# Kernel tuning notes

Hardware: AMD Instinct MI355X
Metric: run time of the kernel (lower is better)

## Reference

```python
import jax, jax.numpy as jnp
import numpy as np

B = 16384          # batch size
NNZ_PER = 32       # active features per position (pieces)
NNZ = B * NNZ_PER
FT_OUT = 512
F_BIG = 49152
F_SMALL = 768
MOD = 640


def setup_inputs() -> dict:
    key = jax.random.key(0)
    ks = jax.random.split(key, 8)
    rows = jnp.repeat(jnp.arange(NNZ // NNZ_PER, dtype=jnp.int64), NNZ_PER)
    stm_cols = jax.random.randint(ks[0], (NNZ,), 0, F_BIG, dtype=jnp.int64)
    nstm_cols = jax.random.randint(ks[1], (NNZ,), 0, F_BIG, dtype=jnp.int64)
    stm_indices = jnp.stack([rows, stm_cols])   # [2, nnz] COO (row, col)
    nstm_indices = jnp.stack([rows, nstm_cols])
    values = jnp.ones((NNZ,), dtype=jnp.float32)
    s = 0.01
    W_ft = jax.random.normal(ks[2], (FT_OUT, F_BIG), dtype=jnp.float32) * s
    b_ft = jax.random.normal(ks[3], (FT_OUT,), dtype=jnp.float32) * s
    W_fft = jax.random.normal(ks[4], (FT_OUT, F_SMALL), dtype=jnp.float32) * s
    b_fft = jax.random.normal(ks[5], (FT_OUT,), dtype=jnp.float32) * s
    W_out = jax.random.normal(ks[6], (1, FT_OUT * 2), dtype=jnp.float32) * s
    b_out = jax.random.normal(ks[7], (1,), dtype=jnp.float32) * s
    return {
        "stm_indices": stm_indices, "nstm_indices": nstm_indices,
        "values": values, "size": B,
        "W_ft": W_ft, "b_ft": b_ft, "W_fft": W_fft, "b_fft": b_fft,
        "W_out": W_out, "b_out": b_out,
    }


def _sparse_linear(indices, values, W, b, size, mod=None):
    # sparse [size, in] @ W.T + b, sparse given as COO (rows, cols, values).
    rows, cols = indices[0], indices[1]
    if mod is not None:
        # faithful to source: `% mod` applied to BOTH row and col indices
        rows = rows % mod
        cols = cols % mod
    contrib = values[:, None] * W.T[cols]            # [nnz, ft_out] gather
    acc = jax.ops.segment_sum(contrib, rows, num_segments=size)
    return acc + b


def reference(stm_indices, nstm_indices, values, size,
              W_ft, b_ft, W_fft, b_fft, W_out, b_out):
    stm_ft = (_sparse_linear(stm_indices, values, W_ft, b_ft, size)
              + _sparse_linear(stm_indices, values, W_fft, b_fft, size, MOD))
    nstm_ft = (_sparse_linear(nstm_indices, values, W_ft, b_ft, size)
               + _sparse_linear(nstm_indices, values, W_fft, b_fft, size, MOD))
    hidden = jnp.clip(jnp.concatenate([stm_ft, nstm_ft], axis=1), 0.0, 1.0)
    return jax.nn.sigmoid(hidden @ W_out.T + b_out)
```

## Files before the change

kernel.cpp:

```cpp
#include <hip/hip_runtime.h>
#include <math.h>

#define B_SZ    16384
#define NNZ_PER 32
#define NNZ     (B_SZ * NNZ_PER)
#define FT_OUT  512
#define F_BIG   49152
#define F_SMALL 768
#define MODV    640

#define TP_A     1536
#define TP_B     80
#define HISTB    (2 * MODV)
#define PREPS_GRID (TP_B + HISTB)

#define NSLICE  16
#define SL_F    32
#define MAIN_GRID (NSLICE * (B_SZ / 4))


__device__ __forceinline__ unsigned short f32_to_bf16_rne(float f) {
    union { float f; unsigned int u; } v; v.f = f;
    unsigned int u = v.u;
    return (unsigned short)((u + 0x7fffu + ((u >> 16) & 1u)) >> 16);
}

__device__ __forceinline__ void unpack_bf16x2(unsigned int u, float& lo, float& hi) {
    union { unsigned int i; float f; } a, b;
    a.i = u << 16;
    b.i = u & 0xffff0000u;
    lo = a.f; hi = b.f;
}

__device__ __forceinline__ float clip01(float x) {
    return fminf(fmaxf(x, 0.0f), 1.0f);
}

__global__ __launch_bounds__(256)
void prep_big(const float* __restrict__ W_ft, unsigned short* __restrict__ Wt) {
    __shared__ __align__(16) unsigned short tA[256][68];
    int b = blockIdx.x;
    int tid = threadIdx.x;
    int ct = b >> 1, ot = b & 1;
    int c0 = ct * 64, o0 = ot * 256;
    int orow = tid >> 4, c4 = (tid & 15) * 4;
#pragma unroll
    for (int it = 0; it < 16; it++) {
        int oo = orow + it * 16;
        float4 f = *(const float4*)(W_ft + (size_t)(o0 + oo) * F_BIG + c0 + c4);
        tA[oo][c4 + 0] = f32_to_bf16_rne(f.x);
        tA[oo][c4 + 1] = f32_to_bf16_rne(f.y);
        tA[oo][c4 + 2] = f32_to_bf16_rne(f.z);
        tA[oo][c4 + 3] = f32_to_bf16_rne(f.w);
    }
    __syncthreads();
    int cc = tid & 63, och = tid >> 6;
    int obase = och * 64;
#pragma unroll
    for (int k = 0; k < 8; k++) {
        int o8 = obase + k * 8;
        uint4 pk;
        pk.x = (unsigned int)tA[o8 + 0][cc] | ((unsigned int)tA[o8 + 1][cc] << 16);
        pk.y = (unsigned int)tA[o8 + 2][cc] | ((unsigned int)tA[o8 + 3][cc] << 16);
        pk.z = (unsigned int)tA[o8 + 4][cc] | ((unsigned int)tA[o8 + 5][cc] << 16);
        pk.w = (unsigned int)tA[o8 + 6][cc] | ((unsigned int)tA[o8 + 7][cc] << 16);
        int og = o0 + o8;
        int s  = og >> 5;
        int f  = og & 31;
        *(uint4*)(Wt + ((size_t)s * F_BIG + (c0 + cc)) * SL_F + f) = pk;
    }
}

__global__ __launch_bounds__(256)
void prep_small(const float* __restrict__ W_fft,
                const int* __restrict__ stm, const int* __restrict__ nstm,
                const float* __restrict__ vals,
                float* __restrict__ Wfft_t, float* __restrict__ H) {
    __shared__ __align__(16) float smem[64 * 65];
    int b = blockIdx.x;
    int tid = threadIdx.x;
    if (b < TP_B) {
        float (*tB)[65] = (float (*)[65])smem;
        int nct = MODV / 64;
        int ot = b / nct, ct = b % nct;
        int c0 = ct * 64, o0 = ot * 64;
        int rr = tid >> 4, c4 = (tid & 15) * 4;
#pragma unroll
        for (int it = 0; it < 4; it++) {
            int oo = rr + it * 16;
            float4 f = *(const float4*)(W_fft + (size_t)(o0 + oo) * F_SMALL + c0 + c4);
            tB[oo][c4 + 0] = f.x; tB[oo][c4 + 1] = f.y;
            tB[oo][c4 + 2] = f.z; tB[oo][c4 + 3] = f.w;
        }
        __syncthreads();
#pragma unroll
        for (int it = 0; it < 4; it++) {
            int idx = tid + it * 256;
            int cc = idx >> 4, g = idx & 15;
            float4 v = make_float4(tB[g * 4 + 0][cc], tB[g * 4 + 1][cc],
                                   tB[g * 4 + 2][cc], tB[g * 4 + 3][cc]);
            *(float4*)(Wfft_t + (size_t)(c0 + cc) * FT_OUT + o0 + g * 4) = v;
        }
    } else {
        float* hrow = smem;
        int hb   = b - TP_B;
        int side = (hb >= MODV) ? 1 : 0;
        int r    = hb - side * MODV;
        const int* cols = (side ? nstm : stm) + NNZ;
        for (int i = tid; i < MODV; i += 256) hrow[i] = 0.0f;
        __syncthreads();
        int nb  = (B_SZ - r + MODV - 1) / MODV;
        int tot = nb * NNZ_PER;
        for (int idx = tid; idx < tot; idx += 256) {
            int j = r * NNZ_PER + (idx >> 5) * (MODV * NNZ_PER) + (idx & 31);
            int c = cols[j] % MODV;
            atomicAdd(&hrow[c], vals[j]);
        }
        __syncthreads();
        float* dst = H + ((size_t)side * MODV + r) * MODV;
        for (int i = tid; i < MODV; i += 256) dst[i] = hrow[i];
    }
}

__global__ __launch_bounds__(512)
void fft_gemm(const float* __restrict__ H, const float* __restrict__ Wfft_t,
              float* __restrict__ acc) {
    __shared__ float hst[MODV][4];
    int o = threadIdx.x;
    int b = blockIdx.x;
    int side = b / 160;
    int s0   = (b % 160) * 4;
    const float* Hs = H + ((size_t)side * MODV + s0) * MODV;
    for (int t = threadIdx.x; t < 4 * MODV; t += 512) {
        int j = t / MODV, cc = t - j * MODV;
        hst[cc][j] = Hs[t];
    }
    __syncthreads();
    float a0 = 0, a1 = 0, a2 = 0, a3 = 0;
    const float* wp = Wfft_t + o;
    for (int cc0 = 0; cc0 < MODV; cc0 += 8) {
        float w[8];
#pragma unroll
        for (int u = 0; u < 8; u++) w[u] = wp[(size_t)(cc0 + u) * FT_OUT];
#pragma unroll
        for (int u = 0; u < 8; u++) {
            float4 hv = *(const float4*)hst[cc0 + u];
            a0 += hv.x * w[u]; a1 += hv.y * w[u];
            a2 += hv.z * w[u]; a3 += hv.w * w[u];
        }
    }
    float* dst = acc + ((size_t)side * MODV + s0) * FT_OUT + o;
    dst[0] = a0; dst[FT_OUT] = a1;
    dst[2 * FT_OUT] = a2; dst[3 * FT_OUT] = a3;
}

__global__ __launch_bounds__(256)
void main_slice(const int* __restrict__ stm, const int* __restrict__ nstm,
                const float* __restrict__ vals,
                const unsigned short* __restrict__ Wt,
                const float* __restrict__ b_ft, const float* __restrict__ b_fft,
                const float* __restrict__ fft_acc,
                const float* __restrict__ W_out, float* __restrict__ partial) {
    int bid   = blockIdx.x;
    int phase = bid >> 15;
    int slice = (bid & 7) + (phase << 3);
    int rowgrp = (bid & 32767) >> 3;
    int tid = threadIdx.x;

    __shared__ int   s_c[4][2][NNZ_PER];
    __shared__ float s_v[4][NNZ_PER];
    {
        int r = tid >> 5, k = tid & 31;
        int row = rowgrp * 4 + (r & 3);
        if (r < 4) {
            s_c[r][0][k] = stm[NNZ + row * NNZ_PER + k];
            s_v[r][k]    = vals[row * NNZ_PER + k];
        } else {
            s_c[r - 4][1][k] = nstm[NNZ + row * NNZ_PER + k];
        }
    }
    __syncthreads();

    int wid  = tid >> 6;
    int lane = tid & 63;
    int row  = rowgrp * 4 + wid;
    int q    = lane >> 4;
    int fp   = lane & 15;

    const unsigned int* ws = (const unsigned int*)Wt + (size_t)slice * F_BIG * 16 + fp;

    float f0 = 0, f1 = 0, g0 = 0, g1 = 0;
#pragma unroll
    for (int kb = 0; kb < 8; kb++) {
        int kk = kb * 4 + q;
        float v = s_v[wid][kk];
        unsigned int w0 = ws[(size_t)s_c[wid][0][kk] * 16];
        unsigned int w1 = ws[(size_t)s_c[wid][1][kk] * 16];
        float lo, hi;
        unpack_bf16x2(w0, lo, hi); f0 += v * lo; f1 += v * hi;
        unpack_bf16x2(w1, lo, hi); g0 += v * lo; g1 += v * hi;
    }
    f0 += __shfl_xor(f0, 16, 64); f0 += __shfl_xor(f0, 32, 64);
    f1 += __shfl_xor(f1, 16, 64); f1 += __shfl_xor(f1, 32, 64);
    g0 += __shfl_xor(g0, 16, 64); g0 += __shfl_xor(g0, 32, 64);
    g1 += __shfl_xor(g1, 16, 64); g1 += __shfl_xor(g1, 32, 64);

    int fo = slice * SL_F + 2 * fp;
    float2 bf  = *(const float2*)(b_ft + fo);
    float2 bb  = *(const float2*)(b_fft + fo);
    float2 wo0 = *(const float2*)(W_out + fo);
    float2 wo1 = *(const float2*)(W_out + FT_OUT + fo);
    float fa0x = 0, fa0y = 0, fa1x = 0, fa1y = 0;
    if (row < MODV) {
        float2 t0 = *(const float2*)(fft_acc + (size_t)row * FT_OUT + fo);
        float2 t1 = *(const float2*)(fft_acc + (size_t)(MODV + row) * FT_OUT + fo);
        fa0x = t0.x; fa0y = t0.y; fa1x = t1.x; fa1y = t1.y;
    }

    float h, dot = 0.0f;
    h = clip01(f0 + bf.x + bb.x + fa0x); dot += h * wo0.x;
    h = clip01(f1 + bf.y + bb.y + fa0y); dot += h * wo0.y;
    h = clip01(g0 + bf.x + bb.x + fa1x); dot += h * wo1.x;
    h = clip01(g1 + bf.y + bb.y + fa1y); dot += h * wo1.y;

#pragma unroll
    for (int off = 32; off > 0; off >>= 1)
        dot += __shfl_down(dot, off, 64);
    if (lane == 0)
        partial[(size_t)slice * B_SZ + row] = dot * 0.25f;
}

__global__ __launch_bounds__(256)
void finish(const float* __restrict__ partial, const float* __restrict__ b_out,
            float* __restrict__ out) {
    int row = blockIdx.x * 256 + threadIdx.x;
    float s = b_out[0];
#pragma unroll
    for (int j = 0; j < NSLICE; j++)
        s += partial[(size_t)j * B_SZ + row];
    out[row] = 1.0f / (1.0f + expf(-s));
}

extern "C" void kernel_launch(void* const* d_in, const int* in_sizes, int n_in,
                              void* d_out, int out_size, void* d_ws, size_t ws_size,
                              hipStream_t stream) {
    const int*   stm   = (const int*)d_in[0];
    const int*   nstm  = (const int*)d_in[1];
    const float* vals  = (const float*)d_in[2];
    const float* W_ft  = (const float*)d_in[4];
    const float* b_ft  = (const float*)d_in[5];
    const float* W_fft = (const float*)d_in[6];
    const float* b_fft = (const float*)d_in[7];
    const float* W_out = (const float*)d_in[8];
    const float* b_out = (const float*)d_in[9];
    float* out = (float*)d_out;

    unsigned short* Wt_bf = (unsigned short*)d_ws;
    float* Wfft_t  = (float*)(Wt_bf + (size_t)F_BIG * FT_OUT);
    float* H       = Wfft_t + (size_t)MODV * FT_OUT;
    float* fft_acc = H + (size_t)2 * MODV * MODV;
    float* partial = fft_acc + (size_t)2 * MODV * FT_OUT;

    prep_small<<<PREPS_GRID, 256, 0, stream>>>(W_fft, stm, nstm, vals, Wfft_t, H);
    fft_gemm<<<320, 512, 0, stream>>>(H, Wfft_t, fft_acc);
    prep_big<<<TP_A, 256, 0, stream>>>(W_ft, Wt_bf);
    main_slice<<<MAIN_GRID, 256, 0, stream>>>(stm, nstm, vals, Wt_bf, b_ft, b_fft,
                                              fft_acc, W_out, partial);
    finish<<<B_SZ / 256, 256, 0, stream>>>(partial, b_out, out);
}
```

Measured before the change: 308.1 us.

## Quantize big weight table to FP8, merge prep kernels, restructure gather and fft GEMM

The big feature-transformer weights are now stored as scaled FP8 instead of bf16, which halves the bytes fetched per gathered column. The main kernel uses 8 slices of 64 features. Each block loops over 16 row groups, double-buffers indices in LDS, issues raw dwordx2 loads and does a transposing shuffle reduction. The two prep kernels are merged into one launch, and the fft GEMM is retiled to 16 rows by 128 outputs per block. FP8 quantization lowers accuracy and may break the tolerance, and the explicit vmcnt(0) wait limits how much load latency can be hidden.

New measurement: 279.6 us. 1.1x faster.

```diff
diff --git a/kernel.cpp b/kernel.cpp
--- a/kernel.cpp
+++ b/kernel.cpp
@@ -12,77 +12,91 @@
 #define TP_A     1536
 #define TP_B     80
 #define HISTB    (2 * MODV)
-#define PREPS_GRID (TP_B + HISTB)
-
-#define NSLICE  16
-#define SL_F    32
-#define MAIN_GRID (NSLICE * (B_SZ / 4))
-
-
-__device__ __forceinline__ unsigned short f32_to_bf16_rne(float f) {
-    union { float f; unsigned int u; } v; v.f = f;
-    unsigned int u = v.u;
-    return (unsigned short)((u + 0x7fffu + ((u >> 16) & 1u)) >> 16);
-}
-
-__device__ __forceinline__ void unpack_bf16x2(unsigned int u, float& lo, float& hi) {
-    union { unsigned int i; float f; } a, b;
-    a.i = u << 16;
-    b.i = u & 0xffff0000u;
-    lo = a.f; hi = b.f;
-}
+#define PREP_GRID (TP_A + TP_B + HISTB)
+
+#define NSLICE  8
+#define SL_F    64
+#define MAIN_G  16
+#define MAIN_GRID (NSLICE * (B_SZ / (4 * MAIN_G)))
+
+#define FFT_SROWS 16
+#define FFT_OQ    128
+#define FFT_BLOCKS (2 * (MODV / FFT_SROWS) * (FT_OUT / FFT_OQ))
+
+#define FP8_SCALE     256.0f
+#define FP8_INV_SCALE 0.00390625f
+
+
+typedef __attribute__((ext_vector_type(2))) float f32x2;
 
 __device__ __forceinline__ float clip01(float x) {
     return fminf(fmaxf(x, 0.0f), 1.0f);
 }
 
+__device__ __forceinline__ unsigned long long gld2(unsigned long long base,
+                                                   unsigned voff) {
+    unsigned long long r;
+    asm volatile("global_load_dwordx2 %0, %1, %2"
+                 : "=v"(r) : "v"(voff), "s"(base));
+    return r;
+}
+
+__device__ __forceinline__ void fma8_fp8(unsigned d0, unsigned d1, float v,
+                                         float* a) {
+    f32x2 p;
+    p = __builtin_amdgcn_cvt_pk_f32_fp8(d0, false); a[0] += v * p.x; a[1] += v * p.y;
+    p = __builtin_amdgcn_cvt_pk_f32_fp8(d0, true);  a[2] += v * p.x; a[3] += v * p.y;
+    p = __builtin_amdgcn_cvt_pk_f32_fp8(d1, false); a[4] += v * p.x; a[5] += v * p.y;
+    p = __builtin_amdgcn_cvt_pk_f32_fp8(d1, true);  a[6] += v * p.x; a[7] += v * p.y;
+}
+
 __global__ __launch_bounds__(256)
-void prep_big(const float* __restrict__ W_ft, unsigned short* __restrict__ Wt) {
-    __shared__ __align__(16) unsigned short tA[256][68];
+void prep_kernel(const float* __restrict__ W_ft, const float* __restrict__ W_fft,
+                 const int* __restrict__ stm, const int* __restrict__ nstm,
+                 const float* __restrict__ vals,
+                 unsigned char* __restrict__ Wt, float* __restrict__ Wfft_t,
+                 float* __restrict__ H) {
+    __shared__ __align__(16) unsigned char smem[256 * 17 * 4];
     int b = blockIdx.x;
     int tid = threadIdx.x;
-    int ct = b >> 1, ot = b & 1;
-    int c0 = ct * 64, o0 = ot * 256;
-    int orow = tid >> 4, c4 = (tid & 15) * 4;
-#pragma unroll
-    for (int it = 0; it < 16; it++) {
-        int oo = orow + it * 16;
-        float4 f = *(const float4*)(W_ft + (size_t)(o0 + oo) * F_BIG + c0 + c4);
-        tA[oo][c4 + 0] = f32_to_bf16_rne(f.x);
-        tA[oo][c4 + 1] = f32_to_bf16_rne(f.y);
-        tA[oo][c4 + 2] = f32_to_bf16_rne(f.z);
-        tA[oo][c4 + 3] = f32_to_bf16_rne(f.w);
-    }
-    __syncthreads();
-    int cc = tid & 63, och = tid >> 6;
-    int obase = och * 64;
-#pragma unroll
-    for (int k = 0; k < 8; k++) {
-        int o8 = obase + k * 8;
-        uint4 pk;
-        pk.x = (unsigned int)tA[o8 + 0][cc] | ((unsigned int)tA[o8 + 1][cc] << 16);
-        pk.y = (unsigned int)tA[o8 + 2][cc] | ((unsigned int)tA[o8 + 3][cc] << 16);
-        pk.z = (unsigned int)tA[o8 + 4][cc] | ((unsigned int)tA[o8 + 5][cc] << 16);
-        pk.w = (unsigned int)tA[o8 + 6][cc] | ((unsigned int)tA[o8 + 7][cc] << 16);
-        int og = o0 + o8;
-        int s  = og >> 5;
-        int f  = og & 31;
-        *(uint4*)(Wt + ((size_t)s * F_BIG + (c0 + cc)) * SL_F + f) = pk;
-    }
-}
-
-__global__ __launch_bounds__(256)
-void prep_small(const float* __restrict__ W_fft,
-                const int* __restrict__ stm, const int* __restrict__ nstm,
-                const float* __restrict__ vals,
-                float* __restrict__ Wfft_t, float* __restrict__ H) {
-    __shared__ __align__(16) float smem[64 * 65];
-    int b = blockIdx.x;
-    int tid = threadIdx.x;
-    if (b < TP_B) {
+    if (b < TP_A) {
+        unsigned (*tA32)[17] = (unsigned (*)[17])smem;
+        int ct = b >> 1, ot = b & 1;
+        int c0 = ct * 64, o0 = ot * 256;
+        int orow = tid >> 4, c4 = (tid & 15) * 4;
+#pragma unroll
+        for (int it = 0; it < 16; it++) {
+            int oo = orow + it * 16;
+            float4 f = *(const float4*)(W_ft + (size_t)(o0 + oo) * F_BIG + c0 + c4);
+            int r = 0;
+            r = __builtin_amdgcn_cvt_pk_fp8_f32(f.x * FP8_SCALE, f.y * FP8_SCALE, r, false);
+            r = __builtin_amdgcn_cvt_pk_fp8_f32(f.z * FP8_SCALE, f.w * FP8_SCALE, r, true);
+            tA32[oo][c4 >> 2] = (unsigned)r;
+        }
+        __syncthreads();
+        int cc = tid >> 2, fs = (tid & 3) * 16;
+        int cw = cc >> 2, cb = (cc & 3) * 8;
+#pragma unroll
+        for (int ss = 0; ss < 4; ss++) {
+            int ob = ss * 64 + fs;
+            unsigned bw[4];
+#pragma unroll
+            for (int w = 0; w < 4; w++) {
+                unsigned e0 = (tA32[ob + 4 * w + 0][cw] >> cb) & 0xffu;
+                unsigned e1 = (tA32[ob + 4 * w + 1][cw] >> cb) & 0xffu;
+                unsigned e2 = (tA32[ob + 4 * w + 2][cw] >> cb) & 0xffu;
+                unsigned e3 = (tA32[ob + 4 * w + 3][cw] >> cb) & 0xffu;
+                bw[w] = e0 | (e1 << 8) | (e2 << 16) | (e3 << 24);
+            }
+            int s = (o0 >> 6) + ss;
+            unsigned char* dst = Wt + ((size_t)s * F_BIG + (c0 + cc)) * SL_F + fs;
+            *(uint4*)dst = make_uint4(bw[0], bw[1], bw[2], bw[3]);
+        }
+    } else if (b < TP_A + TP_B) {
         float (*tB)[65] = (float (*)[65])smem;
+        int b2 = b - TP_A;
         int nct = MODV / 64;
-        int ot = b / nct, ct = b % nct;
+        int ot = b2 / nct, ct = b2 % nct;
         int c0 = ct * 64, o0 = ot * 64;
         int rr = tid >> 4, c4 = (tid & 15) * 4;
 #pragma unroll
@@ -102,8 +116,8 @@
             *(float4*)(Wfft_t + (size_t)(c0 + cc) * FT_OUT + o0 + g * 4) = v;
         }
     } else {
-        float* hrow = smem;
-        int hb   = b - TP_B;
+        float* hrow = (float*)smem;
+        int hb   = b - TP_A - TP_B;
         int side = (hb >= MODV) ? 1 : 0;
         int r    = hb - side * MODV;
         const int* cols = (side ? nstm : stm) + NNZ;
@@ -122,21 +136,25 @@
     }
 }
 
-__global__ __launch_bounds__(512)
+__global__ __launch_bounds__(256)
 void fft_gemm(const float* __restrict__ H, const float* __restrict__ Wfft_t,
               float* __restrict__ acc) {
-    __shared__ float hst[MODV][4];
-    int o = threadIdx.x;
+    __shared__ float hst[FFT_SROWS][MODV];
     int b = blockIdx.x;
-    int side = b / 160;
-    int s0   = (b % 160) * 4;
+    int tid = threadIdx.x;
+    int side  = b / 160;
+    int rem   = b % 160;
+    int s0    = (rem >> 2) * FFT_SROWS;
+    int oq    = rem & 3;
+    int o     = oq * FFT_OQ + (tid & 127);
+    int jh    = (tid >> 7) * 8;
+
     const float* Hs = H + ((size_t)side * MODV + s0) * MODV;
-    for (int t = threadIdx.x; t < 4 * MODV; t += 512) {
-        int j = t / MODV, cc = t - j * MODV;
-        hst[cc][j] = Hs[t];
-    }
+    for (int t = tid; t < FFT_SROWS * MODV; t += 256)
+        ((float*)hst)[t] = Hs[t];
     __syncthreads();
-    float a0 = 0, a1 = 0, a2 = 0, a3 = 0;
+
+    float a[8] = {0, 0, 0, 0, 0, 0, 0, 0};
     const float* wp = Wfft_t + o;
     for (int cc0 = 0; cc0 < MODV; cc0 += 8) {
         float w[8];
@@ -144,90 +162,130 @@
         for (int u = 0; u < 8; u++) w[u] = wp[(size_t)(cc0 + u) * FT_OUT];
 #pragma unroll
         for (int u = 0; u < 8; u++) {
-            float4 hv = *(const float4*)hst[cc0 + u];
-            a0 += hv.x * w[u]; a1 += hv.y * w[u];
-            a2 += hv.z * w[u]; a3 += hv.w * w[u];
+#pragma unroll
+            for (int j = 0; j < 8; j++)
+                a[j] += hst[jh + j][cc0 + u] * w[u];
         }
     }
-    float* dst = acc + ((size_t)side * MODV + s0) * FT_OUT + o;
-    dst[0] = a0; dst[FT_OUT] = a1;
-    dst[2 * FT_OUT] = a2; dst[3 * FT_OUT] = a3;
+    float* dst = acc + ((size_t)side * MODV + s0 + jh) * FT_OUT + o;
+#pragma unroll
+    for (int j = 0; j < 8; j++) dst[(size_t)j * FT_OUT] = a[j];
 }
 
 __global__ __launch_bounds__(256)
 void main_slice(const int* __restrict__ stm, const int* __restrict__ nstm,
                 const float* __restrict__ vals,
-                const unsigned short* __restrict__ Wt,
+                const unsigned char* __restrict__ Wt,
                 const float* __restrict__ b_ft, const float* __restrict__ b_fft,
                 const float* __restrict__ fft_acc,
                 const float* __restrict__ W_out, float* __restrict__ partial) {
-    int bid   = blockIdx.x;
-    int phase = bid >> 15;
-    int slice = (bid & 7) + (phase << 3);
-    int rowgrp = (bid & 32767) >> 3;
+    int bid = blockIdx.x;
+    int slice = bid & 7;
+    int rowbase = (bid >> 3) * (4 * MAIN_G);
     int tid = threadIdx.x;
 
-    __shared__ int   s_c[4][2][NNZ_PER];
-    __shared__ float s_v[4][NNZ_PER];
-    {
-        int r = tid >> 5, k = tid & 31;
-        int row = rowgrp * 4 + (r & 3);
-        if (r < 4) {
-            s_c[r][0][k] = stm[NNZ + row * NNZ_PER + k];
-            s_v[r][k]    = vals[row * NNZ_PER + k];
-        } else {
-            s_c[r - 4][1][k] = nstm[NNZ + row * NNZ_PER + k];
+    __shared__ __align__(16) unsigned s_ct[2][4][2][32];
+    __shared__ __align__(16) float    s_vf[2][4][32];
+
+    int wid = tid >> 6, lane = tid & 63;
+    int q = lane >> 3, fp = lane & 7;
+
+    unsigned long long base =
+        (unsigned long long)(Wt + (size_t)slice * ((size_t)F_BIG * SL_F));
+    unsigned fb = (unsigned)fp * 8u;
+
+    int rS = tid >> 6, sideS = (tid >> 5) & 1, kS = tid & 31;
+    int tkS = (kS & 7) * 4 + (kS >> 3);
+    const int* arrS = sideS ? nstm : stm;
+    int rV = (tid >> 5) & 3, kV = tid & 31;
+    int tkV = (kV & 7) * 4 + (kV >> 3);
+
+    bool b3 = (lane & 8) != 0, b4 = (lane & 16) != 0, b5 = (lane & 32) != 0;
+    int f  = fp * 8 + (b3 ? 4 : 0) + (b4 ? 2 : 0) + (b5 ? 1 : 0);
+    int fo = slice * SL_F + f;
+    float bsum = b_ft[fo] + b_fft[fo];
+    float wo0 = W_out[fo], wo1 = W_out[FT_OUT + fo];
+
+    s_ct[0][rS][sideS][tkS] = (unsigned)arrS[NNZ + (rowbase + rS) * NNZ_PER + kS] << 6;
+    s_vf[0][rV][tkV] = vals[(rowbase + rV) * NNZ_PER + kV] * FP8_INV_SCALE;
+    __syncthreads();
+
+    int cur = 0;
+    for (int g = 0; g < MAIN_G; g++) {
+        int row = rowbase + g * 4 + wid;
+        uint4  cs0 = *(const uint4*)&s_ct[cur][wid][0][q * 4];
+        uint4  cs1 = *(const uint4*)&s_ct[cur][wid][1][q * 4];
+        float4 vf  = *(const float4*)&s_vf[cur][wid][q * 4];
+
+        unsigned long long w00 = gld2(base, cs0.x + fb);
+        unsigned long long w01 = gld2(base, cs0.y + fb);
+        unsigned long long w02 = gld2(base, cs0.z + fb);
+        unsigned long long w03 = gld2(base, cs0.w + fb);
+        unsigned long long w10 = gld2(base, cs1.x + fb);
+        unsigned long long w11 = gld2(base, cs1.y + fb);
+        unsigned long long w12 = gld2(base, cs1.z + fb);
+        unsigned long long w13 = gld2(base, cs1.w + fb);
+
+        float a0[8] = {0, 0, 0, 0, 0, 0, 0, 0};
+        float a1[8] = {0, 0, 0, 0, 0, 0, 0, 0};
+
+        asm volatile("s_waitcnt vmcnt(0)" ::: "memory");
+        __builtin_amdgcn_sched_barrier(0);
+        fma8_fp8((unsigned)w00, (unsigned)(w00 >> 32), vf.x, a0);
+        fma8_fp8((unsigned)w01, (unsigned)(w01 >> 32), vf.y, a0);
+        fma8_fp8((unsigned)w02, (unsigned)(w02 >> 32), vf.z, a0);
+        fma8_fp8((unsigned)w03, (unsigned)(w03 >> 32), vf.w, a0);
+        fma8_fp8((unsigned)w10, (unsigned)(w10 >> 32), vf.x, a1);
+        fma8_fp8((unsigned)w11, (unsigned)(w11 >> 32), vf.y, a1);
+        fma8_fp8((unsigned)w12, (unsigned)(w12 >> 32), vf.z, a1);
+        fma8_fp8((unsigned)w13, (unsigned)(w13 >> 32), vf.w, a1);
+
+        unsigned nc = 0; float nv = 0.0f;
+        if (g + 1 < MAIN_G) {
+            int rn = rowbase + (g + 1) * 4;
+            nc = (unsigned)arrS[NNZ + (rn + rS) * NNZ_PER + kS] << 6;
+            nv = vals[(rn + rV) * NNZ_PER + kV] * FP8_INV_SCALE;
+        }
+
+        float s0[4], s1[4];
+#pragma unroll
+        for (int i = 0; i < 4; i++) {
+            float k0 = b3 ? a0[i + 4] : a0[i], x0 = b3 ? a0[i] : a0[i + 4];
+            float k1 = b3 ? a1[i + 4] : a1[i], x1 = b3 ? a1[i] : a1[i + 4];
+            s0[i] = k0 + __shfl_xor(x0, 8, 64);
+            s1[i] = k1 + __shfl_xor(x1, 8, 64);
+        }
+        float m0[2], m1[2];
+#pragma unroll
+        for (int j = 0; j < 2; j++) {
+            float k0 = b4 ? s0[j + 2] : s0[j], x0 = b4 ? s0[j] : s0[j + 2];
+            float k1 = b4 ? s1[j + 2] : s1[j], x1 = b4 ? s1[j] : s1[j + 2];
+            m0[j] = k0 + __shfl_xor(x0, 16, 64);
+            m1[j] = k1 + __shfl_xor(x1, 16, 64);
+        }
+        float r0 = (b5 ? m0[1] : m0[0]) + __shfl_xor(b5 ? m0[0] : m0[1], 32, 64);
+        float r1 = (b5 ? m1[1] : m1[0]) + __shfl_xor(b5 ? m1[0] : m1[1], 32, 64);
+
+        float fa0 = 0.0f, fa1 = 0.0f;
+        if (row < MODV) {
+            fa0 = fft_acc[(size_t)row * FT_OUT + fo];
+            fa1 = fft_acc[(size_t)(MODV + row) * FT_OUT + fo];
+        }
+        float d = clip01(r0 + bsum + fa0) * wo0 + clip01(r1 + bsum + fa1) * wo1;
+#pragma unroll
+        for (int off = 32; off > 0; off >>= 1)
+            d += __shfl_down(d, off, 64);
+        if (lane == 0)
+            partial[(size_t)slice * B_SZ + row] = d;
+
+        if (g + 1 < MAIN_G) {
+            int nb = cur ^ 1;
+            s_ct[nb][rS][sideS][tkS] = nc;
+            s_vf[nb][rV][tkV] = nv;
+            __syncthreads();
+            cur = nb;
         }
     }
-    __syncthreads();
-
-    int wid  = tid >> 6;
-    int lane = tid & 63;
-    int row  = rowgrp * 4 + wid;
-    int q    = lane >> 4;
-    int fp   = lane & 15;
-
-    const unsigned int* ws = (const unsigned int*)Wt + (size_t)slice * F_BIG * 16 + fp;
-
-    float f0 = 0, f1 = 0, g0 = 0, g1 = 0;
-#pragma unroll
-    for (int kb = 0; kb < 8; kb++) {
-        int kk = kb * 4 + q;
-        float v = s_v[wid][kk];
-        unsigned int w0 = ws[(size_t)s_c[wid][0][kk] * 16];
-        unsigned int w1 = ws[(size_t)s_c[wid][1][kk] * 16];
-        float lo, hi;
-        unpack_bf16x2(w0, lo, hi); f0 += v * lo; f1 += v * hi;
-        unpack_bf16x2(w1, lo, hi); g0 += v * lo; g1 += v * hi;
-    }
-    f0 += __shfl_xor(f0, 16, 64); f0 += __shfl_xor(f0, 32, 64);
-    f1 += __shfl_xor(f1, 16, 64); f1 += __shfl_xor(f1, 32, 64);
-    g0 += __shfl_xor(g0, 16, 64); g0 += __shfl_xor(g0, 32, 64);
-    g1 += __shfl_xor(g1, 16, 64); g1 += __shfl_xor(g1, 32, 64);
-
-    int fo = slice * SL_F + 2 * fp;
-    float2 bf  = *(const float2*)(b_ft + fo);
-    float2 bb  = *(const float2*)(b_fft + fo);
-    float2 wo0 = *(const float2*)(W_out + fo);
-    float2 wo1 = *(const float2*)(W_out + FT_OUT + fo);
-    float fa0x = 0, fa0y = 0, fa1x = 0, fa1y = 0;
-    if (row < MODV) {
-        float2 t0 = *(const float2*)(fft_acc + (size_t)row * FT_OUT + fo);
-        float2 t1 = *(const float2*)(fft_acc + (size_t)(MODV + row) * FT_OUT + fo);
-        fa0x = t0.x; fa0y = t0.y; fa1x = t1.x; fa1y = t1.y;
-    }
-
-    float h, dot = 0.0f;
-    h = clip01(f0 + bf.x + bb.x + fa0x); dot += h * wo0.x;
-    h = clip01(f1 + bf.y + bb.y + fa0y); dot += h * wo0.y;
-    h = clip01(g0 + bf.x + bb.x + fa1x); dot += h * wo1.x;
-    h = clip01(g1 + bf.y + bb.y + fa1y); dot += h * wo1.y;
-
-#pragma unroll
-    for (int off = 32; off > 0; off >>= 1)
-        dot += __shfl_down(dot, off, 64);
-    if (lane == 0)
-        partial[(size_t)slice * B_SZ + row] = dot * 0.25f;
 }
 
 __global__ __launch_bounds__(256)
@@ -255,16 +313,16 @@
     const float* b_out = (const float*)d_in[9];
     float* out = (float*)d_out;
 
-    unsigned short* Wt_bf = (unsigned short*)d_ws;
-    float* Wfft_t  = (float*)(Wt_bf + (size_t)F_BIG * FT_OUT);
+    unsigned char* Wt_f8 = (unsigned char*)d_ws;
+    float* Wfft_t  = (float*)(Wt_f8 + (size_t)F_BIG * FT_OUT);
     float* H       = Wfft_t + (size_t)MODV * FT_OUT;
     float* fft_acc = H + (size_t)2 * MODV * MODV;
     float* partial = fft_acc + (size_t)2 * MODV * FT_OUT;
 
-    prep_small<<<PREPS_GRID, 256, 0, stream>>>(W_fft, stm, nstm, vals, Wfft_t, H);
-    fft_gemm<<<320, 512, 0, stream>>>(H, Wfft_t, fft_acc);
-    prep_big<<<TP_A, 256, 0, stream>>>(W_ft, Wt_bf);
-    main_slice<<<MAIN_GRID, 256, 0, stream>>>(stm, nstm, vals, Wt_bf, b_ft, b_fft,
+    prep_kernel<<<PREP_GRID, 256, 0, stream>>>(W_ft, W_fft, stm, nstm, vals,
+                                               Wt_f8, Wfft_t, H);
+    fft_gemm<<<FFT_BLOCKS, 256, 0, stream>>>(H, Wfft_t, fft_acc);
+    main_slice<<<MAIN_GRID, 256, 0, stream>>>(stm, nstm, vals, Wt_f8, b_ft, b_fft,
                                               fft_acc, W_out, partial);
     finish<<<B_SZ / 256, 256, 0, stream>>>(partial, b_out, out);
 }
```
